# Performance work log

Hardware: AMD Instinct MI355X
Metric: run time of the kernel (lower is better)

The kernel has to match this reference:

```python
import jax, jax.numpy as jnp
import numpy as np

S, D, H, DK, DV = 4096, 1024, 16, 64, 64


def setup_inputs() -> dict:
    key = jax.random.key(0)
    ks = jax.random.split(key, 6)
    x = jax.random.normal(ks[0], (S, D), dtype=jnp.float32)
    # per-head projection weights, stacked over heads; scaled for numerical sanity
    Wq = jax.random.normal(ks[1], (H, D, DK), dtype=jnp.float32) / np.sqrt(D)
    Wk = jax.random.normal(ks[2], (H, D, DK), dtype=jnp.float32) / np.sqrt(D)
    Wv = jax.random.normal(ks[3], (H, D, DV), dtype=jnp.float32) / np.sqrt(D)
    Wc = jax.random.normal(ks[4], (H * DV, D), dtype=jnp.float32) / np.sqrt(H * DV)
    bc = jnp.zeros((D,), dtype=jnp.float32)
    return {"x": x, "Wq": Wq, "Wk": Wk, "Wv": Wv, "Wc": Wc, "bc": bc}


def reference(x, Wq, Wk, Wv, Wc, bc):
    # Per-head projections (original loops over heads with separate Linears;
    # stacking over h is the same math, vectorized).
    q = jnp.einsum("sd,hdk->hsk", x, Wq)   # [H,S,DK]
    k = jnp.einsum("sd,hdk->hsk", x, Wk)   # [H,S,DK]
    v = jnp.einsum("sd,hdv->hsv", x, Wv)   # [H,S,DV]
    scores = jnp.einsum("hsk,htk->hst", q, k) / jnp.sqrt(jnp.asarray(DK, x.dtype))
    probs = jax.nn.softmax(scores, axis=-1)  # softmax over last dim, per row
    o = jnp.einsum("hst,htv->hsv", probs, v)  # [H,S,DV]
    cat = jnp.transpose(o, (1, 0, 2)).reshape(S, H * DV)  # concat heads on last dim
    return cat @ Wc + bc  # output projection with bias
```

## Files before the change

kernel.cpp:

```cpp
#include <hip/hip_runtime.h>
#include <hip/hip_bf16.h>

#define S_ 4096
#define D_ 1024
#define H_ 16
#define DK_ 64
#define DV_ 64

typedef short bf16x8 __attribute__((ext_vector_type(8)));
typedef float floatx4 __attribute__((ext_vector_type(4)));
using bf16 = __hip_bfloat16;

#define MFMA16(a, b, c) __builtin_amdgcn_mfma_f32_16x16x32_bf16(a, b, c, 0, 0, 0)

#if __has_builtin(__builtin_amdgcn_exp2f)
#define EXP2(x) __builtin_amdgcn_exp2f(x)
#else
#define EXP2(x) exp2f(x)
#endif

__device__ __forceinline__ void stage16(const void* g, void* l) {
    __builtin_amdgcn_global_load_lds(
        (const __attribute__((address_space(1))) void*)g,
        (__attribute__((address_space(3))) void*)l, 16, 0, 0);
}

__device__ __forceinline__ bf16x8 ldsfrag(const bf16* base, int row, int chunk) {
    return *(const bf16x8*)(base + row * 64 + (((chunk ^ (row & 7))) << 3));
}

__device__ __forceinline__ unsigned short bfbits(float f) {
    union { bf16 h; unsigned short u; } c; c.h = __float2bfloat16(f); return c.u;
}

__global__ __launch_bounds__(256)
void cvt_x(const float* __restrict__ x, bf16* __restrict__ xb)
{
    int i = (blockIdx.x * 256 + threadIdx.x) * 8;
    float4 a = *(const float4*)(x + i);
    float4 b = *(const float4*)(x + i + 4);
    ushort4 lo, hi;
    lo.x = bfbits(a.x); lo.y = bfbits(a.y); lo.z = bfbits(a.z); lo.w = bfbits(a.w);
    hi.x = bfbits(b.x); hi.y = bfbits(b.y); hi.z = bfbits(b.z); hi.w = bfbits(b.w);
    *(ushort4*)(xb + i) = lo;
    *(ushort4*)(xb + i + 4) = hi;
}

__global__ __launch_bounds__(256)
void tr_qkv(const float* __restrict__ Wq, const float* __restrict__ Wk,
            const float* __restrict__ Wv, bf16* __restrict__ Wt)
{
    const int z = blockIdx.z, which = z >> 4, h = z & 15;
    const float* s = (which == 0 ? Wq : which == 1 ? Wk : Wv) + (size_t)h * D_ * 64;
    bf16* d = Wt + ((size_t)which * 1024 + h * 64) * D_;
    const float scale = (which == 0) ? 0.125f * 1.44269504088896340736f : 1.0f;
    const int r0 = blockIdx.x * 64;
    __shared__ float ls[64][65];
    int t = threadIdx.x;
    {
        int r = t >> 2, cseg = (t & 3) * 16;
        const float* sp = s + (size_t)(r0 + r) * 64 + cseg;
        #pragma unroll
        for (int i = 0; i < 16; i += 4) {
            float4 v = *(const float4*)(sp + i);
            ls[r][cseg + i + 0] = v.x; ls[r][cseg + i + 1] = v.y;
            ls[r][cseg + i + 2] = v.z; ls[r][cseg + i + 3] = v.w;
        }
    }
    __syncthreads();
    {
        int c = t >> 2, rseg = (t & 3) * 16;
        bf16* dp = d + (size_t)c * D_ + r0 + rseg;
        #pragma unroll
        for (int i = 0; i < 16; i++) dp[i] = __float2bfloat16(ls[rseg + i][c] * scale);
    }
}

__global__ __launch_bounds__(256)
void tr_wc(const float* __restrict__ src, bf16* __restrict__ dst)
{
    int r0 = blockIdx.x * 64, c0 = blockIdx.y * 64;
    __shared__ float ls[64][65];
    int t = threadIdx.x;
    {
        int r = t >> 2, cseg = (t & 3) * 16;
        const float* sp = src + (size_t)(r0 + r) * D_ + c0 + cseg;
        #pragma unroll
        for (int i = 0; i < 16; i += 4) {
            float4 v = *(const float4*)(sp + i);
            ls[r][cseg + i + 0] = v.x; ls[r][cseg + i + 1] = v.y;
            ls[r][cseg + i + 2] = v.z; ls[r][cseg + i + 3] = v.w;
        }
    }
    __syncthreads();
    {
        int c = t >> 2, rseg = (t & 3) * 16;
        bf16* dp = dst + (size_t)(c0 + c) * D_ + r0 + rseg;
        #pragma unroll
        for (int i = 0; i < 16; i++) dp[i] = __float2bfloat16(ls[rseg + i][c]);
    }
}

__global__ __launch_bounds__(256)
void qkv_gemm(const bf16* __restrict__ xb, const bf16* __restrict__ Wt,
              bf16* __restrict__ Qb, bf16* __restrict__ Kb, bf16* __restrict__ Vtb)
{
    const int m0 = blockIdx.x * 128;
    const int n0 = blockIdx.y * 128;
    __shared__ __align__(16) bf16 xa[2][128 * 64];
    __shared__ __align__(16) bf16 wb2[2][128 * 64];

    const int t = threadIdx.x, lane = t & 63, w = t >> 6;
    const int l15 = lane & 15, quad = lane >> 4;

    auto stage_a = [&](int buf, int kk) {
        #pragma unroll
        for (int j = 0; j < 4; j++) {
            int c = (j * 4 + w) * 64 + lane;
            int row = c >> 3, ch = (c & 7) ^ (row & 7);
            stage16((const char*)(xb + (size_t)(m0 + row) * D_ + kk) + ch * 16,
                    (char*)&xa[buf][0] + (j * 4 + w) * 1024);
        }
    };
    auto stage_b = [&](int buf, int kk) {
        #pragma unroll
        for (int j = 0; j < 4; j++) {
            int c = (j * 4 + w) * 64 + lane;
            int row = c >> 3, ch = (c & 7) ^ (row & 7);
            stage16((const char*)(Wt + (size_t)(n0 + row) * D_ + kk) + ch * 16,
                    (char*)&wb2[buf][0] + (j * 4 + w) * 1024);
        }
    };

    const floatx4 fz = {0.f, 0.f, 0.f, 0.f};
    floatx4 acc[2][8];
    #pragma unroll
    for (int mt = 0; mt < 2; mt++)
        #pragma unroll
        for (int nt = 0; nt < 8; nt++) acc[mt][nt] = fz;

    stage_a(0, 0); stage_b(0, 0);
    for (int kt = 0; kt < 16; kt++) {
        int cur = kt & 1;
        __syncthreads();
        if (kt < 15) { stage_a(cur ^ 1, (kt + 1) * 64); stage_b(cur ^ 1, (kt + 1) * 64); }
        #pragma unroll
        for (int ks = 0; ks < 2; ks++) {
            bf16x8 a0 = ldsfrag(&xa[cur][0], w * 32 + l15,      ks * 4 + quad);
            bf16x8 a1 = ldsfrag(&xa[cur][0], w * 32 + 16 + l15, ks * 4 + quad);
            #pragma unroll
            for (int nt = 0; nt < 8; nt++) {
                bf16x8 b = ldsfrag(&wb2[cur][0], nt * 16 + l15, ks * 4 + quad);
                acc[0][nt] = MFMA16(a0, b, acc[0][nt]);
                acc[1][nt] = MFMA16(a1, b, acc[1][nt]);
            }
        }
    }

    const int which = n0 >> 10;
    #pragma unroll
    for (int nt = 0; nt < 8; nt++) {
        int n = n0 + nt * 16 + l15;
        int hh = (n >> 6) & 15, col = n & 63;
        #pragma unroll
        for (int mt = 0; mt < 2; mt++)
            #pragma unroll
            for (int r = 0; r < 4; r++) {
                int s = m0 + w * 32 + mt * 16 + quad * 4 + r;
                bf16 val = __float2bfloat16(acc[mt][nt][r]);
                if (which == 0)      Qb[((size_t)hh * S_ + s) * 64 + col] = val;
                else if (which == 1) Kb[((size_t)hh * S_ + s) * 64 + col] = val;
                else                 Vtb[((size_t)hh * 64 + col) * S_ + s] = val;
            }
    }
}

template<int NKT, bool FULL>
__global__ __launch_bounds__(256)
void attn(const bf16* __restrict__ Qb, const bf16* __restrict__ Kb,
          const bf16* __restrict__ Vtb, bf16* __restrict__ Cat,
          float* __restrict__ Opart, float* __restrict__ lpart)
{
    const int m0 = blockIdx.x * 128;
    const int h  = blockIdx.y;
    const int half = blockIdx.z;
    const int keybase = half * (NKT * 64);

    __shared__ __align__(16) bf16 ka[2][64 * 64];
    __shared__ __align__(16) bf16 vt[2][64 * 64];
    __shared__ __align__(16) bf16 pl[128 * 64];
    __shared__ float lsum[128];

    const int t = threadIdx.x, lane = t & 63, w = t >> 6;
    const int l15 = lane & 15, quad = lane >> 4;

    auto stage_kv = [&](int buf, int key0) {
        const char* kg = (const char*)(Kb + ((size_t)h * S_ + key0) * 64);
        #pragma unroll
        for (int j = 0; j < 2; j++) {
            int c = (j * 4 + w) * 64 + lane;
            int row = c >> 3, ch = (c & 7) ^ (row & 7);
            stage16(kg + row * 128 + ch * 16, (char*)&ka[buf][0] + (j * 4 + w) * 1024);
        }
        const char* vg = (const char*)(Vtb + (size_t)h * 64 * S_ + key0);
        #pragma unroll
        for (int j = 0; j < 2; j++) {
            int c = (j * 4 + w) * 64 + lane;
            int row = c >> 3, ch = (c & 7) ^ (row & 7);
            stage16(vg + (size_t)row * (S_ * 2) + ch * 16, (char*)&vt[buf][0] + (j * 4 + w) * 1024);
        }
    };

    bf16x8 qf[2][2];
    #pragma unroll
    for (int nq = 0; nq < 2; nq++)
        #pragma unroll
        for (int ks = 0; ks < 2; ks++)
            qf[nq][ks] = *(const bf16x8*)(Qb +
                ((size_t)h * S_ + m0 + w * 32 + nq * 16 + l15) * 64 + ks * 32 + quad * 8);

    const floatx4 fz = {0.f, 0.f, 0.f, 0.f};
    floatx4 acc[2][4];
    float rs[2] = {0.f, 0.f};
    #pragma unroll
    for (int mt = 0; mt < 2; mt++)
        #pragma unroll
        for (int nt = 0; nt < 4; nt++) acc[mt][nt] = fz;

    stage_kv(0, keybase);
    __syncthreads();

    for (int kt = 0; kt < NKT; kt++) {
        const int cur = kt & 1;
        if (kt + 1 < NKT) stage_kv(cur ^ 1, keybase + (kt + 1) * 64);

        floatx4 sc[4][2];
        #pragma unroll
        for (int mk = 0; mk < 4; mk++)
            #pragma unroll
            for (int nq = 0; nq < 2; nq++) sc[mk][nq] = fz;
        #pragma unroll
        for (int ks = 0; ks < 2; ks++) {
            bf16x8 af[4];
            #pragma unroll
            for (int mk = 0; mk < 4; mk++)
                af[mk] = ldsfrag(&ka[cur][0], mk * 16 + l15, ks * 4 + quad);
            #pragma unroll
            for (int mk = 0; mk < 4; mk++)
                #pragma unroll
                for (int nq = 0; nq < 2; nq++)
                    sc[mk][nq] = MFMA16(af[mk], qf[nq][ks], sc[mk][nq]);
        }

        #pragma unroll
        for (int mk = 0; mk < 4; mk++)
            #pragma unroll
            for (int nq = 0; nq < 2; nq++) {
                float p0 = EXP2(sc[mk][nq][0]);
                float p1 = EXP2(sc[mk][nq][1]);
                float p2 = EXP2(sc[mk][nq][2]);
                float p3 = EXP2(sc[mk][nq][3]);
                rs[nq] += (p0 + p1) + (p2 + p3);
                ushort4 pw;
                pw.x = bfbits(p0); pw.y = bfbits(p1); pw.z = bfbits(p2); pw.w = bfbits(p3);
                int q = w * 32 + nq * 16 + l15;
                int ch = 2 * mk + (quad >> 1);
                *(ushort4*)((char*)pl + q * 128 + ((ch ^ (q & 7)) << 4) + (quad & 1) * 8) = pw;
            }
        asm volatile("s_waitcnt lgkmcnt(0)" ::: "memory");

        #pragma unroll
        for (int ks = 0; ks < 2; ks++) {
            bf16x8 a0 = ldsfrag(pl, w * 32 + l15,      ks * 4 + quad);
            bf16x8 a1 = ldsfrag(pl, w * 32 + 16 + l15, ks * 4 + quad);
            #pragma unroll
            for (int nt = 0; nt < 4; nt++) {
                bf16x8 b = ldsfrag(&vt[cur][0], nt * 16 + l15, ks * 4 + quad);
                acc[0][nt] = MFMA16(a0, b, acc[0][nt]);
                acc[1][nt] = MFMA16(a1, b, acc[1][nt]);
            }
        }
        __syncthreads();
    }

    #pragma unroll
    for (int nq = 0; nq < 2; nq++) {
        rs[nq] += __shfl_xor(rs[nq], 16);
        rs[nq] += __shfl_xor(rs[nq], 32);
        if (quad == 0) lsum[w * 32 + nq * 16 + l15] = rs[nq];
    }
    asm volatile("s_waitcnt lgkmcnt(0)" ::: "memory");

    if (FULL) {
        #pragma unroll
        for (int mt = 0; mt < 2; mt++)
            #pragma unroll
            for (int r = 0; r < 4; r++) {
                int rl = w * 32 + mt * 16 + quad * 4 + r;
                float inv = 1.0f / lsum[rl];
                #pragma unroll
                for (int nt = 0; nt < 4; nt++)
                    Cat[(size_t)(m0 + rl) * (H_ * DV_) + h * 64 + nt * 16 + l15] =
                        __float2bfloat16(acc[mt][nt][r] * inv);
            }
    } else {
        const size_t plane = (size_t)(half * H_ + h) * S_;
        #pragma unroll
        for (int mt = 0; mt < 2; mt++)
            #pragma unroll
            for (int r = 0; r < 4; r++) {
                int rl = w * 32 + mt * 16 + quad * 4 + r;
                #pragma unroll
                for (int nt = 0; nt < 4; nt++)
                    Opart[(plane + m0 + rl) * 64 + nt * 16 + l15] = acc[mt][nt][r];
            }
        #pragma unroll
        for (int nq = 0; nq < 2; nq++)
            if (quad == 0)
                lpart[plane + m0 + w * 32 + nq * 16 + l15] = rs[nq];
    }
}

__global__ __launch_bounds__(256)
void combine(const float* __restrict__ Opart, const float* __restrict__ lpart,
             bf16* __restrict__ Cat)
{
    const int h = blockIdx.y;
    const int off = blockIdx.x * 1024 + threadIdx.x * 4;
    const int s = off >> 6, dv = off & 63;
    float4 o0 = *(const float4*)(Opart + (size_t)h * S_ * 64 + off);
    float4 o1 = *(const float4*)(Opart + (size_t)(H_ + h) * S_ * 64 + off);
    float inv = 1.0f / (lpart[(size_t)h * S_ + s] + lpart[(size_t)(H_ + h) * S_ + s]);
    ushort4 o;
    o.x = bfbits((o0.x + o1.x) * inv);
    o.y = bfbits((o0.y + o1.y) * inv);
    o.z = bfbits((o0.z + o1.z) * inv);
    o.w = bfbits((o0.w + o1.w) * inv);
    *(ushort4*)(Cat + (size_t)s * (H_ * DV_) + h * 64 + dv) = o;
}

__global__ __launch_bounds__(256)
void out_proj(const bf16* __restrict__ Cat, const bf16* __restrict__ Wct,
              const float* __restrict__ bc, float* __restrict__ out)
{
    const int m0 = blockIdx.x * 128;
    const int n0 = blockIdx.y * 64;
    __shared__ __align__(16) bf16 ca[2][128 * 64];
    __shared__ __align__(16) bf16 wb2[2][64 * 64];

    const int t = threadIdx.x, lane = t & 63, w = t >> 6;
    const int l15 = lane & 15, quad = lane >> 4;

    auto stage_a = [&](int buf, int kk) {
        #pragma unroll
        for (int j = 0; j < 4; j++) {
            int c = (j * 4 + w) * 64 + lane;
            int row = c >> 3, ch = (c & 7) ^ (row & 7);
            stage16((const char*)(Cat + (size_t)(m0 + row) * D_ + kk) + ch * 16,
                    (char*)&ca[buf][0] + (j * 4 + w) * 1024);
        }
    };
    auto stage_b = [&](int buf, int kk) {
        #pragma unroll
        for (int j = 0; j < 2; j++) {
            int c = (j * 4 + w) * 64 + lane;
            int row = c >> 3, ch = (c & 7) ^ (row & 7);
            stage16((const char*)(Wct + (size_t)(n0 + row) * D_ + kk) + ch * 16,
                    (char*)&wb2[buf][0] + (j * 4 + w) * 1024);
        }
    };

    const floatx4 fz = {0.f, 0.f, 0.f, 0.f};
    floatx4 acc[2][4];
    #pragma unroll
    for (int mt = 0; mt < 2; mt++)
        #pragma unroll
        for (int nt = 0; nt < 4; nt++) acc[mt][nt] = fz;

    stage_a(0, 0); stage_b(0, 0);
    for (int kt = 0; kt < 16; kt++) {
        int cur = kt & 1;
        __syncthreads();
        if (kt < 15) { stage_a(cur ^ 1, (kt + 1) * 64); stage_b(cur ^ 1, (kt + 1) * 64); }
        #pragma unroll
        for (int ks = 0; ks < 2; ks++) {
            bf16x8 a0 = ldsfrag(&ca[cur][0], w * 32 + l15,      ks * 4 + quad);
            bf16x8 a1 = ldsfrag(&ca[cur][0], w * 32 + 16 + l15, ks * 4 + quad);
            #pragma unroll
            for (int nt = 0; nt < 4; nt++) {
                bf16x8 b = ldsfrag(&wb2[cur][0], nt * 16 + l15, ks * 4 + quad);
                acc[0][nt] = MFMA16(a0, b, acc[0][nt]);
                acc[1][nt] = MFMA16(a1, b, acc[1][nt]);
            }
        }
    }

    #pragma unroll
    for (int nt = 0; nt < 4; nt++) {
        int col = n0 + nt * 16 + l15;
        float bias = bc[col];
        #pragma unroll
        for (int mt = 0; mt < 2; mt++)
            #pragma unroll
            for (int r = 0; r < 4; r++) {
                int row = m0 + w * 32 + mt * 16 + quad * 4 + r;
                out[(size_t)row * D_ + col] = acc[mt][nt][r] + bias;
            }
    }
}

extern "C" void kernel_launch(void* const* d_in, const int* in_sizes, int n_in,
                              void* d_out, int out_size, void* d_ws, size_t ws_size,
                              hipStream_t stream)
{
    const float* x  = (const float*)d_in[0];
    const float* Wq = (const float*)d_in[1];
    const float* Wk = (const float*)d_in[2];
    const float* Wv = (const float*)d_in[3];
    const float* Wc = (const float*)d_in[4];
    const float* bc = (const float*)d_in[5];
    float* out = (float*)d_out;

    bf16* xb  = (bf16*)d_ws;
    bf16* Cat = xb;
    bf16* Wt  = xb  + (size_t)S_ * D_;
    bf16* Wct = Wt  + (size_t)3 * H_ * 64 * D_;
    bf16* Qb  = Wct + (size_t)D_ * H_ * DV_;
    bf16* Kb  = Qb  + (size_t)H_ * S_ * 64;
    bf16* Vtb = Kb  + (size_t)H_ * S_ * 64;
    float* Opart = (float*)(Vtb + (size_t)H_ * 64 * S_);
    float* lpart = Opart + (size_t)2 * H_ * S_ * 64;

    const size_t need_split = (size_t)((char*)(lpart + (size_t)2 * H_ * S_) - (char*)d_ws);
    const bool split = ws_size >= need_split;

    cvt_x<<<dim3(S_ * D_ / (256 * 8)), 256, 0, stream>>>(x, xb);
    tr_qkv<<<dim3(16, 1, 48), 256, 0, stream>>>(Wq, Wk, Wv, Wt);
    tr_wc<<<dim3(16, 16), 256, 0, stream>>>(Wc, Wct);

    qkv_gemm<<<dim3(S_ / 128, 3072 / 128), 256, 0, stream>>>(xb, Wt, Qb, Kb, Vtb);

    if (split) {
        attn<32, false><<<dim3(S_ / 128, H_, 2), 256, 0, stream>>>(
            Qb, Kb, Vtb, Cat, Opart, lpart);
        combine<<<dim3(S_ * 64 / 1024, H_), 256, 0, stream>>>(Opart, lpart, Cat);
    } else {
        attn<64, true><<<dim3(S_ / 128, H_, 1), 256, 0, stream>>>(
            Qb, Kb, Vtb, Cat, Opart, lpart);
    }

    out_proj<<<dim3(S_ / 128, D_ / 64), 256, 0, stream>>>(Cat, Wct, bc, out);
}
```

Baseline: 269.7 us.

## Fuse prep kernels, register-stage GEMM/attention loads, store partials in bf16

Merges the three weight and input conversion kernels into one prep launch to cut launch overhead. Replaces the direct global-to-LDS async loads with register-staged prefetch and a single LDS buffer in qkv_gemm and attn, which halves shared memory and may raise occupancy, but adds an extra barrier per iteration. The split-attention partial outputs are stored as bf16 instead of fp32 to halve their traffic, with the combine kernel widened to 8 elements per thread, at some accuracy cost.

```diff
diff --git a/kernel.cpp b/kernel.cpp
--- a/kernel.cpp
+++ b/kernel.cpp
@@ -19,12 +19,6 @@
 #define EXP2(x) exp2f(x)
 #endif
 
-__device__ __forceinline__ void stage16(const void* g, void* l) {
-    __builtin_amdgcn_global_load_lds(
-        (const __attribute__((address_space(1))) void*)g,
-        (__attribute__((address_space(3))) void*)l, 16, 0, 0);
-}
-
 __device__ __forceinline__ bf16x8 ldsfrag(const bf16* base, int row, int chunk) {
     return *(const bf16x8*)(base + row * 64 + (((chunk ^ (row & 7))) << 3));
 }
@@ -32,72 +26,74 @@
 __device__ __forceinline__ unsigned short bfbits(float f) {
     union { bf16 h; unsigned short u; } c; c.h = __float2bfloat16(f); return c.u;
 }
+__device__ __forceinline__ float bf2f(bf16 h) { return __bfloat162float(h); }
 
 __global__ __launch_bounds__(256)
-void cvt_x(const float* __restrict__ x, bf16* __restrict__ xb)
-{
-    int i = (blockIdx.x * 256 + threadIdx.x) * 8;
-    float4 a = *(const float4*)(x + i);
-    float4 b = *(const float4*)(x + i + 4);
-    ushort4 lo, hi;
-    lo.x = bfbits(a.x); lo.y = bfbits(a.y); lo.z = bfbits(a.z); lo.w = bfbits(a.w);
-    hi.x = bfbits(b.x); hi.y = bfbits(b.y); hi.z = bfbits(b.z); hi.w = bfbits(b.w);
-    *(ushort4*)(xb + i) = lo;
-    *(ushort4*)(xb + i + 4) = hi;
-}
-
-__global__ __launch_bounds__(256)
-void tr_qkv(const float* __restrict__ Wq, const float* __restrict__ Wk,
-            const float* __restrict__ Wv, bf16* __restrict__ Wt)
-{
-    const int z = blockIdx.z, which = z >> 4, h = z & 15;
-    const float* s = (which == 0 ? Wq : which == 1 ? Wk : Wv) + (size_t)h * D_ * 64;
-    bf16* d = Wt + ((size_t)which * 1024 + h * 64) * D_;
-    const float scale = (which == 0) ? 0.125f * 1.44269504088896340736f : 1.0f;
-    const int r0 = blockIdx.x * 64;
+void prep(const float* __restrict__ x, const float* __restrict__ Wq,
+          const float* __restrict__ Wk, const float* __restrict__ Wv,
+          const float* __restrict__ Wc,
+          bf16* __restrict__ xb, bf16* __restrict__ Wt, bf16* __restrict__ Wct)
+{
     __shared__ float ls[64][65];
-    int t = threadIdx.x;
+    const int bx = blockIdx.x, t = threadIdx.x;
+
+    if (bx < 2048) {
+        int i = bx * 2048 + t * 8;
+        float4 a = *(const float4*)(x + i);
+        float4 b = *(const float4*)(x + i + 4);
+        ushort4 lo, hi;
+        lo.x = bfbits(a.x); lo.y = bfbits(a.y); lo.z = bfbits(a.z); lo.w = bfbits(a.w);
+        hi.x = bfbits(b.x); hi.y = bfbits(b.y); hi.z = bfbits(b.z); hi.w = bfbits(b.w);
+        *(ushort4*)(xb + i) = lo;
+        *(ushort4*)(xb + i + 4) = hi;
+        return;
+    }
+    if (bx < 2816) {
+        const int idx = bx - 2048;
+        const int z = idx >> 4, which = z >> 4, h = z & 15;
+        const float* s = (which == 0 ? Wq : which == 1 ? Wk : Wv) + (size_t)h * D_ * 64;
+        bf16* d = Wt + ((size_t)which * 1024 + h * 64) * D_;
+        const float scale = (which == 0) ? 0.125f * 1.44269504088896340736f : 1.0f;
+        const int r0 = (idx & 15) * 64;
+        {
+            int r = t >> 2, cseg = (t & 3) * 16;
+            const float* sp = s + (size_t)(r0 + r) * 64 + cseg;
+            #pragma unroll
+            for (int i = 0; i < 16; i += 4) {
+                float4 v = *(const float4*)(sp + i);
+                ls[r][cseg + i + 0] = v.x; ls[r][cseg + i + 1] = v.y;
+                ls[r][cseg + i + 2] = v.z; ls[r][cseg + i + 3] = v.w;
+            }
+        }
+        __syncthreads();
+        {
+            int c = t >> 2, rseg = (t & 3) * 16;
+            bf16* dp = d + (size_t)c * D_ + r0 + rseg;
+            #pragma unroll
+            for (int i = 0; i < 16; i++) dp[i] = __float2bfloat16(ls[rseg + i][c] * scale);
+        }
+        return;
+    }
     {
-        int r = t >> 2, cseg = (t & 3) * 16;
-        const float* sp = s + (size_t)(r0 + r) * 64 + cseg;
-        #pragma unroll
-        for (int i = 0; i < 16; i += 4) {
-            float4 v = *(const float4*)(sp + i);
-            ls[r][cseg + i + 0] = v.x; ls[r][cseg + i + 1] = v.y;
-            ls[r][cseg + i + 2] = v.z; ls[r][cseg + i + 3] = v.w;
-        }
-    }
-    __syncthreads();
-    {
-        int c = t >> 2, rseg = (t & 3) * 16;
-        bf16* dp = d + (size_t)c * D_ + r0 + rseg;
-        #pragma unroll
-        for (int i = 0; i < 16; i++) dp[i] = __float2bfloat16(ls[rseg + i][c] * scale);
-    }
-}
-
-__global__ __launch_bounds__(256)
-void tr_wc(const float* __restrict__ src, bf16* __restrict__ dst)
-{
-    int r0 = blockIdx.x * 64, c0 = blockIdx.y * 64;
-    __shared__ float ls[64][65];
-    int t = threadIdx.x;
-    {
-        int r = t >> 2, cseg = (t & 3) * 16;
-        const float* sp = src + (size_t)(r0 + r) * D_ + c0 + cseg;
-        #pragma unroll
-        for (int i = 0; i < 16; i += 4) {
-            float4 v = *(const float4*)(sp + i);
-            ls[r][cseg + i + 0] = v.x; ls[r][cseg + i + 1] = v.y;
-            ls[r][cseg + i + 2] = v.z; ls[r][cseg + i + 3] = v.w;
-        }
-    }
-    __syncthreads();
-    {
-        int c = t >> 2, rseg = (t & 3) * 16;
-        bf16* dp = dst + (size_t)(c0 + c) * D_ + r0 + rseg;
-        #pragma unroll
-        for (int i = 0; i < 16; i++) dp[i] = __float2bfloat16(ls[rseg + i][c]);
+        const int idx = bx - 2816;
+        const int r0 = (idx & 15) * 64, c0 = (idx >> 4) * 64;
+        {
+            int r = t >> 2, cseg = (t & 3) * 16;
+            const float* sp = Wc + (size_t)(r0 + r) * D_ + c0 + cseg;
+            #pragma unroll
+            for (int i = 0; i < 16; i += 4) {
+                float4 v = *(const float4*)(sp + i);
+                ls[r][cseg + i + 0] = v.x; ls[r][cseg + i + 1] = v.y;
+                ls[r][cseg + i + 2] = v.z; ls[r][cseg + i + 3] = v.w;
+            }
+        }
+        __syncthreads();
+        {
+            int c = t >> 2, rseg = (t & 3) * 16;
+            bf16* dp = Wct + (size_t)(c0 + c) * D_ + r0 + rseg;
+            #pragma unroll
+            for (int i = 0; i < 16; i++) dp[i] = __float2bfloat16(ls[rseg + i][c]);
+        }
     }
 }
 
@@ -107,28 +103,31 @@
 {
     const int m0 = blockIdx.x * 128;
     const int n0 = blockIdx.y * 128;
-    __shared__ __align__(16) bf16 xa[2][128 * 64];
-    __shared__ __align__(16) bf16 wb2[2][128 * 64];
+    __shared__ __align__(16) bf16 xa[128 * 64];
+    __shared__ __align__(16) bf16 wb2[128 * 64];
 
     const int t = threadIdx.x, lane = t & 63, w = t >> 6;
     const int l15 = lane & 15, quad = lane >> 4;
 
-    auto stage_a = [&](int buf, int kk) {
+    const int prow = t >> 3, pch = t & 7;
+    const int lds_off = prow * 128 + ((pch ^ (prow & 7)) << 4);
+
+    int4 pa[4], pb[4];
+    auto loadAB = [&](int kk) {
         #pragma unroll
         for (int j = 0; j < 4; j++) {
-            int c = (j * 4 + w) * 64 + lane;
-            int row = c >> 3, ch = (c & 7) ^ (row & 7);
-            stage16((const char*)(xb + (size_t)(m0 + row) * D_ + kk) + ch * 16,
-                    (char*)&xa[buf][0] + (j * 4 + w) * 1024);
-        }
-    };
-    auto stage_b = [&](int buf, int kk) {
+            int row = j * 32 + prow;
+            pa[j] = *(const int4*)((const char*)xb +
+                     ((size_t)(m0 + row) * D_ + kk) * 2 + pch * 16);
+            pb[j] = *(const int4*)((const char*)Wt +
+                     ((size_t)(n0 + row) * D_ + kk) * 2 + pch * 16);
+        }
+    };
+    auto writeAB = [&]() {
         #pragma unroll
         for (int j = 0; j < 4; j++) {
-            int c = (j * 4 + w) * 64 + lane;
-            int row = c >> 3, ch = (c & 7) ^ (row & 7);
-            stage16((const char*)(Wt + (size_t)(n0 + row) * D_ + kk) + ch * 16,
-                    (char*)&wb2[buf][0] + (j * 4 + w) * 1024);
+            *(int4*)((char*)xa + j * 4096 + lds_off)  = pa[j];
+            *(int4*)((char*)wb2 + j * 4096 + lds_off) = pb[j];
         }
     };
 
@@ -139,21 +138,26 @@
         #pragma unroll
         for (int nt = 0; nt < 8; nt++) acc[mt][nt] = fz;
 
-    stage_a(0, 0); stage_b(0, 0);
+    loadAB(0);
+    writeAB();
+    __syncthreads();
     for (int kt = 0; kt < 16; kt++) {
-        int cur = kt & 1;
-        __syncthreads();
-        if (kt < 15) { stage_a(cur ^ 1, (kt + 1) * 64); stage_b(cur ^ 1, (kt + 1) * 64); }
+        if (kt < 15) loadAB((kt + 1) * 64);
         #pragma unroll
         for (int ks = 0; ks < 2; ks++) {
-            bf16x8 a0 = ldsfrag(&xa[cur][0], w * 32 + l15,      ks * 4 + quad);
-            bf16x8 a1 = ldsfrag(&xa[cur][0], w * 32 + 16 + l15, ks * 4 + quad);
+            bf16x8 a0 = ldsfrag(xa, w * 32 + l15,      ks * 4 + quad);
+            bf16x8 a1 = ldsfrag(xa, w * 32 + 16 + l15, ks * 4 + quad);
             #pragma unroll
             for (int nt = 0; nt < 8; nt++) {
-                bf16x8 b = ldsfrag(&wb2[cur][0], nt * 16 + l15, ks * 4 + quad);
+                bf16x8 b = ldsfrag(wb2, nt * 16 + l15, ks * 4 + quad);
                 acc[0][nt] = MFMA16(a0, b, acc[0][nt]);
                 acc[1][nt] = MFMA16(a1, b, acc[1][nt]);
             }
+        }
+        __syncthreads();
+        if (kt < 15) {
+            writeAB();
+            __syncthreads();
         }
     }
 
@@ -179,36 +183,38 @@
 __global__ __launch_bounds__(256)
 void attn(const bf16* __restrict__ Qb, const bf16* __restrict__ Kb,
           const bf16* __restrict__ Vtb, bf16* __restrict__ Cat,
-          float* __restrict__ Opart, float* __restrict__ lpart)
+          bf16* __restrict__ Opart, float* __restrict__ lpart)
 {
     const int m0 = blockIdx.x * 128;
     const int h  = blockIdx.y;
     const int half = blockIdx.z;
     const int keybase = half * (NKT * 64);
 
-    __shared__ __align__(16) bf16 ka[2][64 * 64];
-    __shared__ __align__(16) bf16 vt[2][64 * 64];
+    __shared__ __align__(16) bf16 ka[64 * 64];
+    __shared__ __align__(16) bf16 vt[64 * 64];
     __shared__ __align__(16) bf16 pl[128 * 64];
     __shared__ float lsum[128];
 
     const int t = threadIdx.x, lane = t & 63, w = t >> 6;
     const int l15 = lane & 15, quad = lane >> 4;
 
-    auto stage_kv = [&](int buf, int key0) {
+    const int prow = t >> 3, pch = t & 7;
+    const int lds_off = prow * 128 + ((pch ^ (prow & 7)) << 4);
+
+    int4 pk[2], pv[2];
+    auto load_kv = [&](int key0) {
         const char* kg = (const char*)(Kb + ((size_t)h * S_ + key0) * 64);
-        #pragma unroll
-        for (int j = 0; j < 2; j++) {
-            int c = (j * 4 + w) * 64 + lane;
-            int row = c >> 3, ch = (c & 7) ^ (row & 7);
-            stage16(kg + row * 128 + ch * 16, (char*)&ka[buf][0] + (j * 4 + w) * 1024);
-        }
+        pk[0] = *(const int4*)(kg + (size_t)prow * 128 + pch * 16);
+        pk[1] = *(const int4*)(kg + (size_t)(prow + 32) * 128 + pch * 16);
         const char* vg = (const char*)(Vtb + (size_t)h * 64 * S_ + key0);
-        #pragma unroll
-        for (int j = 0; j < 2; j++) {
-            int c = (j * 4 + w) * 64 + lane;
-            int row = c >> 3, ch = (c & 7) ^ (row & 7);
-            stage16(vg + (size_t)row * (S_ * 2) + ch * 16, (char*)&vt[buf][0] + (j * 4 + w) * 1024);
-        }
+        pv[0] = *(const int4*)(vg + (size_t)prow * (S_ * 2) + pch * 16);
+        pv[1] = *(const int4*)(vg + (size_t)(prow + 32) * (S_ * 2) + pch * 16);
+    };
+    auto write_kv = [&]() {
+        *(int4*)((char*)ka + lds_off)        = pk[0];
+        *(int4*)((char*)ka + 4096 + lds_off) = pk[1];
+        *(int4*)((char*)vt + lds_off)        = pv[0];
+        *(int4*)((char*)vt + 4096 + lds_off) = pv[1];
     };
 
     bf16x8 qf[2][2];
@@ -227,12 +233,12 @@
         #pragma unroll
         for (int nt = 0; nt < 4; nt++) acc[mt][nt] = fz;
 
-    stage_kv(0, keybase);
+    load_kv(keybase);
+    write_kv();
     __syncthreads();
 
     for (int kt = 0; kt < NKT; kt++) {
-        const int cur = kt & 1;
-        if (kt + 1 < NKT) stage_kv(cur ^ 1, keybase + (kt + 1) * 64);
+        if (kt + 1 < NKT) load_kv(keybase + (kt + 1) * 64);
 
         floatx4 sc[4][2];
         #pragma unroll
@@ -244,7 +250,7 @@
             bf16x8 af[4];
             #pragma unroll
             for (int mk = 0; mk < 4; mk++)
-                af[mk] = ldsfrag(&ka[cur][0], mk * 16 + l15, ks * 4 + quad);
+                af[mk] = ldsfrag(ka, mk * 16 + l15, ks * 4 + quad);
             #pragma unroll
             for (int mk = 0; mk < 4; mk++)
                 #pragma unroll
@@ -275,12 +281,16 @@
             bf16x8 a1 = ldsfrag(pl, w * 32 + 16 + l15, ks * 4 + quad);
             #pragma unroll
             for (int nt = 0; nt < 4; nt++) {
-                bf16x8 b = ldsfrag(&vt[cur][0], nt * 16 + l15, ks * 4 + quad);
+                bf16x8 b = ldsfrag(vt, nt * 16 + l15, ks * 4 + quad);
                 acc[0][nt] = MFMA16(a0, b, acc[0][nt]);
                 acc[1][nt] = MFMA16(a1, b, acc[1][nt]);
             }
         }
         __syncthreads();
+        if (kt + 1 < NKT) {
+            write_kv();
+            __syncthreads();
+        }
     }
 
     #pragma unroll
@@ -312,7 +322,8 @@
                 int rl = w * 32 + mt * 16 + quad * 4 + r;
                 #pragma unroll
                 for (int nt = 0; nt < 4; nt++)
-                    Opart[(plane + m0 + rl) * 64 + nt * 16 + l15] = acc[mt][nt][r];
+                    Opart[(plane + m0 + rl) * 64 + nt * 16 + l15] =
+                        __float2bfloat16(acc[mt][nt][r]);
             }
         #pragma unroll
         for (int nq = 0; nq < 2; nq++)
@@ -322,21 +333,26 @@
 }
 
 __global__ __launch_bounds__(256)
-void combine(const float* __restrict__ Opart, const float* __restrict__ lpart,
+void combine(const bf16* __restrict__ Opart, const float* __restrict__ lpart,
              bf16* __restrict__ Cat)
 {
     const int h = blockIdx.y;
-    const int off = blockIdx.x * 1024 + threadIdx.x * 4;
+    const int off = (blockIdx.x * 256 + threadIdx.x) * 8;
     const int s = off >> 6, dv = off & 63;
-    float4 o0 = *(const float4*)(Opart + (size_t)h * S_ * 64 + off);
-    float4 o1 = *(const float4*)(Opart + (size_t)(H_ + h) * S_ * 64 + off);
+    union { bf16x8 v; bf16 e[8]; } o0, o1, o;
+    o0.v = *(const bf16x8*)(Opart + (size_t)h * S_ * 64 + off);
+    o1.v = *(const bf16x8*)(Opart + (size_t)(H_ + h) * S_ * 64 + off);
     float inv = 1.0f / (lpart[(size_t)h * S_ + s] + lpart[(size_t)(H_ + h) * S_ + s]);
-    ushort4 o;
-    o.x = bfbits((o0.x + o1.x) * inv);
-    o.y = bfbits((o0.y + o1.y) * inv);
-    o.z = bfbits((o0.z + o1.z) * inv);
-    o.w = bfbits((o0.w + o1.w) * inv);
-    *(ushort4*)(Cat + (size_t)s * (H_ * DV_) + h * 64 + dv) = o;
+    #pragma unroll
+    for (int i = 0; i < 8; i++)
+        o.e[i] = __float2bfloat16((bf2f(o0.e[i]) + bf2f(o1.e[i])) * inv);
+    *(bf16x8*)(Cat + (size_t)s * (H_ * DV_) + h * 64 + dv) = o.v;
+}
+
+__device__ __forceinline__ void stage16(const void* g, void* l) {
+    __builtin_amdgcn_global_load_lds(
+        (const __attribute__((address_space(1))) void*)g,
+        (__attribute__((address_space(3))) void*)l, 16, 0, 0);
 }
 
 __global__ __launch_bounds__(256)
@@ -428,22 +444,19 @@
     bf16* Qb  = Wct + (size_t)D_ * H_ * DV_;
     bf16* Kb  = Qb  + (size_t)H_ * S_ * 64;
     bf16* Vtb = Kb  + (size_t)H_ * S_ * 64;
-    float* Opart = (float*)(Vtb + (size_t)H_ * 64 * S_);
-    float* lpart = Opart + (size_t)2 * H_ * S_ * 64;
+    bf16* Opart = Vtb + (size_t)H_ * 64 * S_;
+    float* lpart = (float*)(Opart + (size_t)2 * H_ * S_ * 64);
 
     const size_t need_split = (size_t)((char*)(lpart + (size_t)2 * H_ * S_) - (char*)d_ws);
     const bool split = ws_size >= need_split;
 
-    cvt_x<<<dim3(S_ * D_ / (256 * 8)), 256, 0, stream>>>(x, xb);
-    tr_qkv<<<dim3(16, 1, 48), 256, 0, stream>>>(Wq, Wk, Wv, Wt);
-    tr_wc<<<dim3(16, 16), 256, 0, stream>>>(Wc, Wct);
-
+    prep<<<dim3(3072), 256, 0, stream>>>(x, Wq, Wk, Wv, Wc, xb, Wt, Wct);
     qkv_gemm<<<dim3(S_ / 128, 3072 / 128), 256, 0, stream>>>(xb, Wt, Qb, Kb, Vtb);
 
     if (split) {
         attn<32, false><<<dim3(S_ / 128, H_, 2), 256, 0, stream>>>(
             Qb, Kb, Vtb, Cat, Opart, lpart);
-        combine<<<dim3(S_ * 64 / 1024, H_), 256, 0, stream>>>(Opart, lpart, Cat);
+        combine<<<dim3(S_ * 64 / 2048, H_), 256, 0, stream>>>(Opart, lpart, Cat);
     } else {
         attn<64, true><<<dim3(S_ / 128, H_, 1), 256, 0, stream>>>(
             Qb, Kb, Vtb, Cat, Opart, lpart);
```

New measurement: 379.6 us. 40.7% more time.

## Merge prep kernels and halve attention P-tile LDS for higher occupancy

Applied to the files above, without the earlier changes.

Folds the x conversion and the two weight-transpose kernels into one prep launch, removing two kernel launches and the gaps between them. In attention, the 64-key tile is handled in two 32-key halves. The P buffer in LDS shrinks to 128x32 with a new swizzle, lsum reuses that buffer, and launch_bounds requests 4 blocks per CU. This aims to cut LDS and register use so more attention blocks fit per CU. The cost is more waits and serialization per key tile.

```diff
diff --git a/kernel.cpp b/kernel.cpp
--- a/kernel.cpp
+++ b/kernel.cpp
@@ -34,70 +34,71 @@
 }
 
 __global__ __launch_bounds__(256)
-void cvt_x(const float* __restrict__ x, bf16* __restrict__ xb)
-{
-    int i = (blockIdx.x * 256 + threadIdx.x) * 8;
-    float4 a = *(const float4*)(x + i);
-    float4 b = *(const float4*)(x + i + 4);
-    ushort4 lo, hi;
-    lo.x = bfbits(a.x); lo.y = bfbits(a.y); lo.z = bfbits(a.z); lo.w = bfbits(a.w);
-    hi.x = bfbits(b.x); hi.y = bfbits(b.y); hi.z = bfbits(b.z); hi.w = bfbits(b.w);
-    *(ushort4*)(xb + i) = lo;
-    *(ushort4*)(xb + i + 4) = hi;
-}
-
-__global__ __launch_bounds__(256)
-void tr_qkv(const float* __restrict__ Wq, const float* __restrict__ Wk,
-            const float* __restrict__ Wv, bf16* __restrict__ Wt)
-{
-    const int z = blockIdx.z, which = z >> 4, h = z & 15;
-    const float* s = (which == 0 ? Wq : which == 1 ? Wk : Wv) + (size_t)h * D_ * 64;
-    bf16* d = Wt + ((size_t)which * 1024 + h * 64) * D_;
-    const float scale = (which == 0) ? 0.125f * 1.44269504088896340736f : 1.0f;
-    const int r0 = blockIdx.x * 64;
+void prep(const float* __restrict__ x, const float* __restrict__ Wq,
+          const float* __restrict__ Wk, const float* __restrict__ Wv,
+          const float* __restrict__ Wc,
+          bf16* __restrict__ xb, bf16* __restrict__ Wt, bf16* __restrict__ Wct)
+{
     __shared__ float ls[64][65];
-    int t = threadIdx.x;
+    const int bx = blockIdx.x, t = threadIdx.x;
+
+    if (bx < 2048) {
+        int i = bx * 2048 + t * 8;
+        float4 a = *(const float4*)(x + i);
+        float4 b = *(const float4*)(x + i + 4);
+        ushort4 lo, hi;
+        lo.x = bfbits(a.x); lo.y = bfbits(a.y); lo.z = bfbits(a.z); lo.w = bfbits(a.w);
+        hi.x = bfbits(b.x); hi.y = bfbits(b.y); hi.z = bfbits(b.z); hi.w = bfbits(b.w);
+        *(ushort4*)(xb + i) = lo;
+        *(ushort4*)(xb + i + 4) = hi;
+        return;
+    }
+    if (bx < 2816) {
+        const int idx = bx - 2048;
+        const int z = idx >> 4, which = z >> 4, h = z & 15;
+        const float* s = (which == 0 ? Wq : which == 1 ? Wk : Wv) + (size_t)h * D_ * 64;
+        bf16* d = Wt + ((size_t)which * 1024 + h * 64) * D_;
+        const float scale = (which == 0) ? 0.125f * 1.44269504088896340736f : 1.0f;
+        const int r0 = (idx & 15) * 64;
+        {
+            int r = t >> 2, cseg = (t & 3) * 16;
+            const float* sp = s + (size_t)(r0 + r) * 64 + cseg;
+            #pragma unroll
+            for (int i = 0; i < 16; i += 4) {
+                float4 v = *(const float4*)(sp + i);
+                ls[r][cseg + i + 0] = v.x; ls[r][cseg + i + 1] = v.y;
+                ls[r][cseg + i + 2] = v.z; ls[r][cseg + i + 3] = v.w;
+            }
+        }
+        __syncthreads();
+        {
+            int c = t >> 2, rseg = (t & 3) * 16;
+            bf16* dp = d + (size_t)c * D_ + r0 + rseg;
+            #pragma unroll
+            for (int i = 0; i < 16; i++) dp[i] = __float2bfloat16(ls[rseg + i][c] * scale);
+        }
+        return;
+    }
     {
-        int r = t >> 2, cseg = (t & 3) * 16;
-        const float* sp = s + (size_t)(r0 + r) * 64 + cseg;
-        #pragma unroll
-        for (int i = 0; i < 16; i += 4) {
-            float4 v = *(const float4*)(sp + i);
-            ls[r][cseg + i + 0] = v.x; ls[r][cseg + i + 1] = v.y;
-            ls[r][cseg + i + 2] = v.z; ls[r][cseg + i + 3] = v.w;
-        }
-    }
-    __syncthreads();
-    {
-        int c = t >> 2, rseg = (t & 3) * 16;
-        bf16* dp = d + (size_t)c * D_ + r0 + rseg;
-        #pragma unroll
-        for (int i = 0; i < 16; i++) dp[i] = __float2bfloat16(ls[rseg + i][c] * scale);
-    }
-}
-
-__global__ __launch_bounds__(256)
-void tr_wc(const float* __restrict__ src, bf16* __restrict__ dst)
-{
-    int r0 = blockIdx.x * 64, c0 = blockIdx.y * 64;
-    __shared__ float ls[64][65];
-    int t = threadIdx.x;
-    {
-        int r = t >> 2, cseg = (t & 3) * 16;
-        const float* sp = src + (size_t)(r0 + r) * D_ + c0 + cseg;
-        #pragma unroll
-        for (int i = 0; i < 16; i += 4) {
-            float4 v = *(const float4*)(sp + i);
-            ls[r][cseg + i + 0] = v.x; ls[r][cseg + i + 1] = v.y;
-            ls[r][cseg + i + 2] = v.z; ls[r][cseg + i + 3] = v.w;
-        }
-    }
-    __syncthreads();
-    {
-        int c = t >> 2, rseg = (t & 3) * 16;
-        bf16* dp = dst + (size_t)(c0 + c) * D_ + r0 + rseg;
-        #pragma unroll
-        for (int i = 0; i < 16; i++) dp[i] = __float2bfloat16(ls[rseg + i][c]);
+        const int idx = bx - 2816;
+        const int r0 = (idx & 15) * 64, c0 = (idx >> 4) * 64;
+        {
+            int r = t >> 2, cseg = (t & 3) * 16;
+            const float* sp = Wc + (size_t)(r0 + r) * D_ + c0 + cseg;
+            #pragma unroll
+            for (int i = 0; i < 16; i += 4) {
+                float4 v = *(const float4*)(sp + i);
+                ls[r][cseg + i + 0] = v.x; ls[r][cseg + i + 1] = v.y;
+                ls[r][cseg + i + 2] = v.z; ls[r][cseg + i + 3] = v.w;
+            }
+        }
+        __syncthreads();
+        {
+            int c = t >> 2, rseg = (t & 3) * 16;
+            bf16* dp = Wct + (size_t)(c0 + c) * D_ + r0 + rseg;
+            #pragma unroll
+            for (int i = 0; i < 16; i++) dp[i] = __float2bfloat16(ls[rseg + i][c]);
+        }
     }
 }
 
@@ -176,7 +177,7 @@
 }
 
 template<int NKT, bool FULL>
-__global__ __launch_bounds__(256)
+__global__ __launch_bounds__(256, 4)
 void attn(const bf16* __restrict__ Qb, const bf16* __restrict__ Kb,
           const bf16* __restrict__ Vtb, bf16* __restrict__ Cat,
           float* __restrict__ Opart, float* __restrict__ lpart)
@@ -188,8 +189,7 @@
 
     __shared__ __align__(16) bf16 ka[2][64 * 64];
     __shared__ __align__(16) bf16 vt[2][64 * 64];
-    __shared__ __align__(16) bf16 pl[128 * 64];
-    __shared__ float lsum[128];
+    __shared__ __align__(16) bf16 pl[128 * 32];
 
     const int t = threadIdx.x, lane = t & 63, w = t >> 6;
     const int l15 = lane & 15, quad = lane >> 4;
@@ -227,6 +227,10 @@
         #pragma unroll
         for (int nt = 0; nt < 4; nt++) acc[mt][nt] = fz;
 
+    const int fq = (l15 >> 2) & 3;
+    const int prd0 = (w * 32 + l15) * 64 + ((quad ^ fq) << 4);
+    const int prd1 = (w * 32 + 16 + l15) * 64 + ((quad ^ fq) << 4);
+
     stage_kv(0, keybase);
     __syncthreads();
 
@@ -234,48 +238,47 @@
         const int cur = kt & 1;
         if (kt + 1 < NKT) stage_kv(cur ^ 1, keybase + (kt + 1) * 64);
 
-        floatx4 sc[4][2];
-        #pragma unroll
-        for (int mk = 0; mk < 4; mk++)
-            #pragma unroll
-            for (int nq = 0; nq < 2; nq++) sc[mk][nq] = fz;
-        #pragma unroll
-        for (int ks = 0; ks < 2; ks++) {
-            bf16x8 af[4];
-            #pragma unroll
-            for (int mk = 0; mk < 4; mk++)
-                af[mk] = ldsfrag(&ka[cur][0], mk * 16 + l15, ks * 4 + quad);
-            #pragma unroll
-            for (int mk = 0; mk < 4; mk++)
+        #pragma unroll
+        for (int hf = 0; hf < 2; hf++) {
+            floatx4 sc[2][2];
+            #pragma unroll
+            for (int mk = 0; mk < 2; mk++)
                 #pragma unroll
-                for (int nq = 0; nq < 2; nq++)
-                    sc[mk][nq] = MFMA16(af[mk], qf[nq][ks], sc[mk][nq]);
-        }
-
-        #pragma unroll
-        for (int mk = 0; mk < 4; mk++)
-            #pragma unroll
-            for (int nq = 0; nq < 2; nq++) {
-                float p0 = EXP2(sc[mk][nq][0]);
-                float p1 = EXP2(sc[mk][nq][1]);
-                float p2 = EXP2(sc[mk][nq][2]);
-                float p3 = EXP2(sc[mk][nq][3]);
-                rs[nq] += (p0 + p1) + (p2 + p3);
-                ushort4 pw;
-                pw.x = bfbits(p0); pw.y = bfbits(p1); pw.z = bfbits(p2); pw.w = bfbits(p3);
-                int q = w * 32 + nq * 16 + l15;
-                int ch = 2 * mk + (quad >> 1);
-                *(ushort4*)((char*)pl + q * 128 + ((ch ^ (q & 7)) << 4) + (quad & 1) * 8) = pw;
-            }
-        asm volatile("s_waitcnt lgkmcnt(0)" ::: "memory");
-
-        #pragma unroll
-        for (int ks = 0; ks < 2; ks++) {
-            bf16x8 a0 = ldsfrag(pl, w * 32 + l15,      ks * 4 + quad);
-            bf16x8 a1 = ldsfrag(pl, w * 32 + 16 + l15, ks * 4 + quad);
+                for (int nq = 0; nq < 2; nq++) sc[mk][nq] = fz;
+            #pragma unroll
+            for (int ks = 0; ks < 2; ks++) {
+                bf16x8 af0 = ldsfrag(&ka[cur][0], (hf * 2 + 0) * 16 + l15, ks * 4 + quad);
+                bf16x8 af1 = ldsfrag(&ka[cur][0], (hf * 2 + 1) * 16 + l15, ks * 4 + quad);
+                #pragma unroll
+                for (int nq = 0; nq < 2; nq++) {
+                    sc[0][nq] = MFMA16(af0, qf[nq][ks], sc[0][nq]);
+                    sc[1][nq] = MFMA16(af1, qf[nq][ks], sc[1][nq]);
+                }
+            }
+
+            #pragma unroll
+            for (int mk = 0; mk < 2; mk++)
+                #pragma unroll
+                for (int nq = 0; nq < 2; nq++) {
+                    float p0 = EXP2(sc[mk][nq][0]);
+                    float p1 = EXP2(sc[mk][nq][1]);
+                    float p2 = EXP2(sc[mk][nq][2]);
+                    float p3 = EXP2(sc[mk][nq][3]);
+                    rs[nq] += (p0 + p1) + (p2 + p3);
+                    ushort4 pw;
+                    pw.x = bfbits(p0); pw.y = bfbits(p1); pw.z = bfbits(p2); pw.w = bfbits(p3);
+                    int q = w * 32 + nq * 16 + l15;
+                    int ch = mk * 2 + (quad >> 1);
+                    *(ushort4*)((char*)pl + q * 64 + ((ch ^ ((q >> 2) & 3)) << 4)
+                                + (quad & 1) * 8) = pw;
+                }
+            asm volatile("s_waitcnt lgkmcnt(0)" ::: "memory");
+
+            bf16x8 a0 = *(const bf16x8*)((const char*)pl + prd0);
+            bf16x8 a1 = *(const bf16x8*)((const char*)pl + prd1);
             #pragma unroll
             for (int nt = 0; nt < 4; nt++) {
-                bf16x8 b = ldsfrag(&vt[cur][0], nt * 16 + l15, ks * 4 + quad);
+                bf16x8 b = ldsfrag(&vt[cur][0], nt * 16 + l15, hf * 4 + quad);
                 acc[0][nt] = MFMA16(a0, b, acc[0][nt]);
                 acc[1][nt] = MFMA16(a1, b, acc[1][nt]);
             }
@@ -283,6 +286,8 @@
         __syncthreads();
     }
 
+    __syncthreads();
+    float* lsum = (float*)pl;
     #pragma unroll
     for (int nq = 0; nq < 2; nq++) {
         rs[nq] += __shfl_xor(rs[nq], 16);
@@ -434,10 +439,7 @@
     const size_t need_split = (size_t)((char*)(lpart + (size_t)2 * H_ * S_) - (char*)d_ws);
     const bool split = ws_size >= need_split;
 
-    cvt_x<<<dim3(S_ * D_ / (256 * 8)), 256, 0, stream>>>(x, xb);
-    tr_qkv<<<dim3(16, 1, 48), 256, 0, stream>>>(Wq, Wk, Wv, Wt);
-    tr_wc<<<dim3(16, 16), 256, 0, stream>>>(Wc, Wct);
-
+    prep<<<dim3(3072), 256, 0, stream>>>(x, Wq, Wk, Wv, Wc, xb, Wt, Wct);
     qkv_gemm<<<dim3(S_ / 128, 3072 / 128), 256, 0, stream>>>(xb, Wt, Qb, Kb, Vtb);
 
     if (split) {
```

Result: faster. 246.8 us (-8.5%).
